# Kernel tuning notes

Hardware: AMD Instinct MI355X
Metric: run time of the kernel (lower is better)

## Reference

```python
import jax, jax.numpy as jnp
import numpy as np

BATCH_SIZE = 64
NUM_DISTORT = 24
NUM_LEVEL = 5
FEAT = 2048
N_ROWS = BATCH_SIZE * NUM_DISTORT * NUM_LEVEL  # 7680


def _pair_indices():
    # Faithful reproduction of the original quadruple loop's indexing:
    #   rows inputs[batch*distort + i] vs inputs[batch*distort + j],
    #   i in [0, L-2], j in [i, L-1].
    bases = (np.arange(BATCH_SIZE)[:, None] * np.arange(NUM_DISTORT)[None, :]).reshape(-1)  # [B*D]
    ii, jj = [], []
    for i in range(NUM_LEVEL - 1):
        for j in range(i, NUM_LEVEL):
            ii.append(i)
            jj.append(j)
    ii = np.asarray(ii)  # [P], P = L(L+1)/2 - 1 = 14
    jj = np.asarray(jj)
    I = (bases[:, None] + ii[None, :]).reshape(-1)  # [B*D*P]
    J = (bases[:, None] + jj[None, :]).reshape(-1)
    return jnp.asarray(I, dtype=jnp.int32), jnp.asarray(J, dtype=jnp.int32)


def setup_inputs() -> dict:
    key = jax.random.key(0)
    inputs = jax.random.normal(key, (N_ROWS, FEAT), dtype=jnp.float32)
    return {"inputs": inputs}


def reference(inputs):
    I, J = _pair_indices()
    # gather both sides of every margin pair, hinge at 0, reduce to scalar
    diff = inputs[I] - inputs[J]  # [B*D*P, FEAT]
    return jnp.sum(jnp.maximum(diff, 0.0))
```

## Files before the change

kernel.cpp:

```cpp
#include <hip/hip_runtime.h>

#define FEAT 2048
#define CH 16
#define COLSPLIT 4
#define THREADS 128

struct Tables {
    int nchunk;
    short r0[1456];
    float W[1472][4];
};

constexpr Tables make_tables() {
    Tables t{};
    int cnt[1450] = {};
    for (int b = 0; b < 64; ++b)
        for (int d = 0; d < 24; ++d)
            cnt[b * d]++;
    for (int r = 0; r < 1472; ++r)
        for (int dl = 1; dl <= 4; ++dl) {
            int s = 0;
            for (int i = 0; i <= 4 - dl; ++i) {
                int v = r - i;
                if (v >= 0 && v < 1450) s += cnt[v];
            }
            t.W[r][dl - 1] = (float)s;
        }
    t.nchunk = 0;
    int r = 0;
    while (r < 1453) {
        bool act = false;
        for (int i = 0; i <= 3; ++i) {
            int v = r - i;
            if (v >= 0 && v < 1450 && cnt[v] > 0) act = true;
        }
        if (act) { t.r0[t.nchunk++] = (short)r; r += CH; }
        else ++r;
    }
    return t;
}

constexpr Tables TBL = make_tables();
constexpr int NCHUNK = TBL.nchunk;
constexpr int NPART  = NCHUNK * COLSPLIT;

__constant__ Tables d_tbl = make_tables();

__global__ __launch_bounds__(THREADS) void hinge_rows(const float* __restrict__ in,
                                                      float* __restrict__ partial) {
    const int chunk = blockIdx.x / COLSPLIT;
    const int chalf = blockIdx.x % COLSPLIT;
    const int r0    = d_tbl.r0[chunk];
    const float* p  = in + (long)r0 * FEAT + chalf * (FEAT / COLSPLIT) + threadIdx.x * 4;

    float4 x[5];
    #pragma unroll
    for (int l = 0; l < 4; ++l)
        x[l] = *(const float4*)(p + l * FEAT);

    float acc0 = 0.f, acc1 = 0.f;
    #pragma unroll
    for (int k = 0; k < CH; ++k) {
        x[4] = *(const float4*)(p + (k + 4) * FEAT);
        #pragma unroll
        for (int dl = 1; dl <= 4; ++dl) {
            const float w = d_tbl.W[r0 + k][dl - 1];
            float s = fmaxf(x[0].x - x[dl].x, 0.f)
                    + fmaxf(x[0].y - x[dl].y, 0.f)
                    + fmaxf(x[0].z - x[dl].z, 0.f)
                    + fmaxf(x[0].w - x[dl].w, 0.f);
            if (dl & 1) acc0 = fmaf(w, s, acc0);
            else        acc1 = fmaf(w, s, acc1);
        }
        #pragma unroll
        for (int l = 0; l < 4; ++l) x[l] = x[l + 1];
    }

    float acc = acc0 + acc1;
    #pragma unroll
    for (int off = 32; off > 0; off >>= 1)
        acc += __shfl_down(acc, off, 64);

    __shared__ float ws2[THREADS / 64];
    const int lane = threadIdx.x & 63, wave = threadIdx.x >> 6;
    if (lane == 0) ws2[wave] = acc;
    __syncthreads();
    if (threadIdx.x == 0) partial[blockIdx.x] = ws2[0] + ws2[1];
}

__global__ __launch_bounds__(256) void reduce_final(const float* __restrict__ partial,
                                                    float* __restrict__ out) {
    const int t = threadIdx.x;
    float acc = 0.f;
    for (int i = t; i < NPART; i += 256) acc += partial[i];

    #pragma unroll
    for (int off = 32; off > 0; off >>= 1)
        acc += __shfl_down(acc, off, 64);

    __shared__ float ws[4];
    const int lane = t & 63, wave = t >> 6;
    if (lane == 0) ws[wave] = acc;
    __syncthreads();
    if (t == 0) out[0] = (ws[0] + ws[1]) + (ws[2] + ws[3]);
}

extern "C" void kernel_launch(void* const* d_in, const int* in_sizes, int n_in,
                              void* d_out, int out_size, void* d_ws, size_t ws_size,
                              hipStream_t stream) {
    const float* in  = (const float*)d_in[0];
    float* out       = (float*)d_out;
    float* partial   = (float*)d_ws;

    hinge_rows<<<NPART, THREADS, 0, stream>>>(in, partial);
    reduce_final<<<1, 256, 0, stream>>>(partial, out);
}
```

Measured before the change: 10.96 us.

## Use single-wave blocks with shorter row chunks and load all rows upfront

Switches the hinge kernel to one 64-thread wave per block, 8 column parts and 8-row chunks, so there are many more blocks and the cross-wave shared-memory reduction and barrier go away. All CH+4 row loads are issued at the start rather than streamed one per step, giving more memory-level parallelism per thread at the cost of more registers. The final reduction reads the partials as float4. Shorter chunks mean a larger fraction of rows are re-read as halo (12 loads per 8 rows instead of 20 per 16), and the float4 read assumes NPART is a multiple of 4 and the partial buffer is 16-byte aligned.

```diff
diff --git a/kernel.cpp b/kernel.cpp
--- a/kernel.cpp
+++ b/kernel.cpp
@@ -1,9 +1,10 @@
 #include <hip/hip_runtime.h>
 
 #define FEAT 2048
-#define CH 16
-#define COLSPLIT 4
-#define THREADS 128
+#define CH 8
+#define COLSPLIT 8
+#define THREADS 64
+#define NROWS_LD (CH + 4)
 
 struct Tables {
     int nchunk;
@@ -48,32 +49,29 @@
 
 __global__ __launch_bounds__(THREADS) void hinge_rows(const float* __restrict__ in,
                                                       float* __restrict__ partial) {
-    const int chunk = blockIdx.x / COLSPLIT;
-    const int chalf = blockIdx.x % COLSPLIT;
+    const int chunk = blockIdx.x >> 3;
+    const int cpart = blockIdx.x & 7;
     const int r0    = d_tbl.r0[chunk];
-    const float* p  = in + (long)r0 * FEAT + chalf * (FEAT / COLSPLIT) + threadIdx.x * 4;
+    const float* p  = in + (long)r0 * FEAT + cpart * (FEAT / COLSPLIT) + threadIdx.x * 4;
 
-    float4 x[5];
+    float4 x[NROWS_LD];
     #pragma unroll
-    for (int l = 0; l < 4; ++l)
+    for (int l = 0; l < NROWS_LD; ++l)
         x[l] = *(const float4*)(p + l * FEAT);
 
     float acc0 = 0.f, acc1 = 0.f;
     #pragma unroll
     for (int k = 0; k < CH; ++k) {
-        x[4] = *(const float4*)(p + (k + 4) * FEAT);
         #pragma unroll
         for (int dl = 1; dl <= 4; ++dl) {
             const float w = d_tbl.W[r0 + k][dl - 1];
-            float s = fmaxf(x[0].x - x[dl].x, 0.f)
-                    + fmaxf(x[0].y - x[dl].y, 0.f)
-                    + fmaxf(x[0].z - x[dl].z, 0.f)
-                    + fmaxf(x[0].w - x[dl].w, 0.f);
+            float s = fmaxf(x[k].x - x[k + dl].x, 0.f)
+                    + fmaxf(x[k].y - x[k + dl].y, 0.f)
+                    + fmaxf(x[k].z - x[k + dl].z, 0.f)
+                    + fmaxf(x[k].w - x[k + dl].w, 0.f);
             if (dl & 1) acc0 = fmaf(w, s, acc0);
             else        acc1 = fmaf(w, s, acc1);
         }
-        #pragma unroll
-        for (int l = 0; l < 4; ++l) x[l] = x[l + 1];
     }
 
     float acc = acc0 + acc1;
@@ -81,18 +79,18 @@
     for (int off = 32; off > 0; off >>= 1)
         acc += __shfl_down(acc, off, 64);
 
-    __shared__ float ws2[THREADS / 64];
-    const int lane = threadIdx.x & 63, wave = threadIdx.x >> 6;
-    if (lane == 0) ws2[wave] = acc;
-    __syncthreads();
-    if (threadIdx.x == 0) partial[blockIdx.x] = ws2[0] + ws2[1];
+    if (threadIdx.x == 0) partial[blockIdx.x] = acc;
 }
 
 __global__ __launch_bounds__(256) void reduce_final(const float* __restrict__ partial,
                                                     float* __restrict__ out) {
     const int t = threadIdx.x;
+    constexpr int NV4 = NPART / 4;
     float acc = 0.f;
-    for (int i = t; i < NPART; i += 256) acc += partial[i];
+    for (int i = t; i < NV4; i += 256) {
+        float4 v = ((const float4*)partial)[i];
+        acc += (v.x + v.y) + (v.z + v.w);
+    }
 
     #pragma unroll
     for (int off = 32; off > 0; off >>= 1)
```

Result: no change. 10.95 us (median of 3 runs) (-0.1%).
